# Performance work log

Measured on AMD Instinct MI355X. Metric: run time of the kernel, lower is better.

The kernel has to match this reference:

```python
import jax, jax.numpy as jnp
import numpy as np

N, IN_DIM, HIDDEN, OUT_DIM, K = 16384, 64, 128, 128, 32


def setup_inputs() -> dict:
    key = jax.random.key(0)
    k1, k2, k3 = jax.random.split(key, 3)
    x = jax.random.normal(k1, (N, IN_DIM), dtype=jnp.float32)
    std1 = 1.0 / np.sqrt(2 * IN_DIM)
    w = jax.random.uniform(k2, (HIDDEN, 2 * IN_DIM), dtype=jnp.float32, minval=-std1, maxval=std1)
    std2 = 1.0 / np.sqrt(IN_DIM + HIDDEN)
    w2 = jax.random.uniform(k3, (OUT_DIM, IN_DIM + HIDDEN), dtype=jnp.float32, minval=-std2, maxval=std2)
    return {"x": x, "w": w, "w2": w2, "k": K}


def reference(x, w, w2, k):
    # kNN graph via squared euclidean distances (same ordering as torch.norm cdist)
    sq = jnp.sum(x * x, axis=-1)                      # (N,)
    d2 = sq[:, None] + sq[None, :] - 2.0 * (x @ x.T)  # (N, N)
    _, graph = jax.lax.top_k(-d2, k)                  # (N, k) indices of k smallest distances
    # gather neighbor features and concat broadcast self features
    nb = x[graph]                                      # (N, k, in_dim)
    self_rep = jnp.broadcast_to(x[:, None, :], nb.shape)
    feat = jnp.concatenate([nb, self_rep], axis=-1)    # (N, k, 2*in_dim)
    # linear + Hardtanh + average pooling over neighborhood
    h = jnp.clip(jnp.einsum('nkf,hf->nkh', feat, w), -1.0, 1.0)
    pooled = h.mean(axis=1)                            # (N, hidden)
    # second linear on [pooled, x]
    out = jnp.concatenate([pooled, x], axis=-1) @ w2.T # (N, out_dim)
    return out
```

## Files before the change

### kernel.cpp

```cpp
#include <hip/hip_runtime.h>

#define NPTS   16384
#define IN_DIM 64
#define HID    128
#define KSEL   32

#define CAP    128
#define TRIG   64
#define WIN_HI 48
#define SLACK  0.30f
#define INFBITS 0x7f800000u

typedef _Float16 f16x8 __attribute__((ext_vector_type(8)));
typedef float    f32x4 __attribute__((ext_vector_type(4)));
typedef unsigned short u16;
typedef unsigned int   u32;
typedef unsigned long long u64;

__global__ __launch_bounds__(256) void prep_kernel(const float* __restrict__ x,
                                                   float* __restrict__ sq,
                                                   u16* __restrict__ ph,
                                                   u16* __restrict__ pl) {
    const int i  = blockIdx.x * 256 + threadIdx.x;
    const int ct = i >> 4, li = i & 15;
    const float4* xr = (const float4*)(x + (size_t)i * IN_DIM);
    float s = 0.f;
#pragma unroll
    for (int c = 0; c < 8; ++c) {
        float4 a = xr[2 * c], b = xr[2 * c + 1];
        float e[8] = {a.x, a.y, a.z, a.w, b.x, b.y, b.z, b.w};
        u32 hw[8], lw[8];
#pragma unroll
        for (int j = 0; j < 8; ++j) {
            s += e[j] * e[j];
            _Float16 h = (_Float16)e[j];
            float hf = (float)h;
            _Float16 l = (_Float16)(e[j] - hf);
            hw[j] = __builtin_bit_cast(u16, h);
            lw[j] = __builtin_bit_cast(u16, l);
        }
        size_t off = ((size_t)ct * 8 + c) * 128 + (size_t)li * 8;
        *(uint4*)(ph + off) = make_uint4(hw[0] | (hw[1] << 16), hw[2] | (hw[3] << 16),
                                         hw[4] | (hw[5] << 16), hw[6] | (hw[7] << 16));
        *(uint4*)(pl + off) = make_uint4(lw[0] | (lw[1] << 16), lw[2] | (lw[3] << 16),
                                         lw[4] | (lw[5] << 16), lw[6] | (lw[7] << 16));
    }
    sq[i] = s;
}

__device__ __forceinline__ void compact_row(float* bdrow, u16* bjrow, int* pcnt,
                                            u32* pthr, int lane) {
    int n = *pcnt; n = n < CAP ? n : CAP;
    const float INF = __int_as_float(INFBITS);
    float dv0 = (lane      < n) ? bdrow[lane]      : INF;
    float dv1 = (lane + 64 < n) ? bdrow[lane + 64] : INF;
    u16   jv0 = (lane      < n) ? bjrow[lane]      : 0;
    u16   jv1 = (lane + 64 < n) ? bjrow[lane + 64] : 0;
    u32 u0 = __float_as_uint(dv0), u1 = __float_as_uint(dv1);
    u32 lo = 0, hi = *pthr, ans = hi;
    for (int it = 0; it < 26 && lo < hi; ++it) {
        u32 mid = lo + ((hi - lo) >> 1);
        int c = __popcll(__ballot(u0 <= mid)) + __popcll(__ballot(u1 <= mid));
        if (c < 32) lo = mid + 1;
        else { hi = mid; ans = mid; if (c <= WIN_HI) break; }
    }
    float ansf = __uint_as_float(ans) + SLACK;
    u64 mlt = (1ull << lane) - 1ull;
    bool p0 = dv0 <= ansf;
    u64 b0 = __ballot(p0);
    if (p0) { int p = __popcll(b0 & mlt); bdrow[p] = dv0; bjrow[p] = jv0; }
    int base = __popcll(b0);
    bool p1 = dv1 <= ansf;
    u64 b1 = __ballot(p1);
    if (p1) { int p = base + __popcll(b1 & mlt); if (p < CAP) { bdrow[p] = dv1; bjrow[p] = jv1; } }
    base += __popcll(b1);
    if (lane == 0) {
        *pcnt = base < CAP ? base : CAP;
        atomicMin(pthr, __float_as_uint(ansf));
    }
}

__global__ __launch_bounds__(256, 3) void knn_kernel(const float* __restrict__ x,
                                                     const u16* __restrict__ ph,
                                                     const u16* __restrict__ pl,
                                                     const float* __restrict__ sq,
                                                     int* __restrict__ graph) {
    __shared__ float bd[4][16][CAP];
    __shared__ u16   bj[4][16][CAP];
    __shared__ int   bcnt[4][16];
    __shared__ u32   bthrU[16];

    const int t = threadIdx.x, lane = t & 63, wave = t >> 6;
    const int g = lane >> 4, li = lane & 15;
    const int rg = blockIdx.x;
    const int rbase = rg * 16;

    if (t < 64) bcnt[t >> 4][t & 15] = 0;
    if (t < 16) bthrU[t] = INFBITS;

    f16x8 ah[2], al[2];
#pragma unroll
    for (int kh = 0; kh < 2; ++kh) {
        size_t o = ((size_t)rg * 2 + kh) * 512 + (size_t)lane * 8;
        ah[kh] = *(const f16x8*)(ph + o);
        al[kh] = *(const f16x8*)(pl + o);
    }
    float sar[4];
#pragma unroll
    for (int r = 0; r < 4; ++r) sar[r] = sq[rbase + g * 4 + r];
    __syncthreads();

    int ctb = wave * 4;
    f16x8 cb[4][2]; float csb[4];
#pragma unroll
    for (int c = 0; c < 4; ++c) {
        size_t o = (size_t)(ctb + c) * 1024 + (size_t)lane * 8;
        cb[c][0] = *(const f16x8*)(ph + o);
        cb[c][1] = *(const f16x8*)(ph + o + 512);
        csb[c] = sq[(ctb + c) * 16 + li];
    }

    for (int i = 0; i < 64; ++i) {
        const int nctb = ctb + 16;
        f16x8 nb[4][2]; float nsb[4];
        if (i < 63) {
#pragma unroll
            for (int c = 0; c < 4; ++c) {
                size_t o = (size_t)(nctb + c) * 1024 + (size_t)lane * 8;
                nb[c][0] = *(const f16x8*)(ph + o);
                nb[c][1] = *(const f16x8*)(ph + o + 512);
                nsb[c] = sq[(nctb + c) * 16 + li];
            }
        }
        f32x4 acc[4];
#pragma unroll
        for (int c = 0; c < 4; ++c) {
            f32x4 a = {0.f, 0.f, 0.f, 0.f};
            a = __builtin_amdgcn_mfma_f32_16x16x32_f16(ah[0], cb[c][0], a, 0, 0, 0);
            a = __builtin_amdgcn_mfma_f32_16x16x32_f16(ah[1], cb[c][1], a, 0, 0, 0);
            a = __builtin_amdgcn_mfma_f32_16x16x32_f16(al[0], cb[c][0], a, 0, 0, 0);
            a = __builtin_amdgcn_mfma_f32_16x16x32_f16(al[1], cb[c][1], a, 0, 0, 0);
            acc[c] = a;
        }
        uint4 tu = *(const uint4*)&bthrU[g * 4];
        const float thr[4] = {__uint_as_float(tu.x), __uint_as_float(tu.y),
                              __uint_as_float(tu.z), __uint_as_float(tu.w)};
#pragma unroll
        for (int c = 0; c < 4; ++c) {
#pragma unroll
            for (int r = 0; r < 4; ++r) {
                float d = fmaf(-2.f, acc[c][r], sar[r] + csb[c]);
                bool pred = d <= thr[r];
                if (__any(pred)) {
                    if (pred) {
                        int row = g * 4 + r;
                        int pos = atomicAdd(&bcnt[wave][row], 1);
                        if (pos < CAP) {
                            bd[wave][row][pos] = fmaxf(d, 0.f);
                            bj[wave][row][pos] = (u16)((ctb + c) * 16 + li);
                        }
                    }
                }
            }
        }
        u64 need = __ballot((lane < 16) && (bcnt[wave][lane] > TRIG));
        while (need) {
            int rr = __ffsll((long long)need) - 1;
            need &= need - 1;
            compact_row(bd[wave][rr], bj[wave][rr], &bcnt[wave][rr], &bthrU[rr], lane);
        }
        ctb = nctb;
#pragma unroll
        for (int c = 0; c < 4; ++c) { cb[c][0] = nb[c][0]; cb[c][1] = nb[c][1]; csb[c] = nsb[c]; }
    }

    __syncthreads();

    const u64 mlt = (1ull << lane) - 1ull;
    for (int ii = 0; ii < 4; ++ii) {
        const int lr = wave * 4 + ii;
        const int gr = rbase + lr;
        const float sqa = sq[gr];
        const float4* xa = (const float4*)(x + (size_t)gr * IN_DIM);
        int ns[4];
#pragma unroll
        for (int s = 0; s < 4; ++s) { int v = bcnt[s][lr]; ns[s] = v < CAP ? v : CAP; }
        u32 db[8]; int jj[8];
#pragma unroll
        for (int s8 = 0; s8 < 8; ++s8) {
            const int sl = s8 >> 1;
            const int half = s8 & 1;
            u32 dbits = INFBITS; int j = 0;
            if (ns[sl] > half * 64) {
                int idx = half * 64 + lane;
                if (idx < ns[sl]) {
                    j = bj[sl][lr][idx];
                    const float4* xb = (const float4*)(x + (size_t)j * IN_DIM);
                    float dot = 0.f;
#pragma unroll
                    for (int q = 0; q < 16; ++q) {
                        float4 a = xa[q], b = xb[q];
                        dot += a.x * b.x + a.y * b.y + a.z * b.z + a.w * b.w;
                    }
                    float d = fmaxf(fmaf(-2.f, dot, sqa + sq[j]), 0.f);
                    dbits = __float_as_uint(d);
                }
            }
            db[s8] = dbits; jj[s8] = j;
        }
        u32 lo = 0, hi = INFBITS, ans = hi;
        for (int it = 0; it < 32 && lo < hi; ++it) {
            u32 mid = lo + ((hi - lo) >> 1);
            int c = 0;
#pragma unroll
            for (int s8 = 0; s8 < 8; ++s8)
                c += __popcll(__ballot(db[s8] <= mid));
            if (c < 32) lo = mid + 1;
            else { hi = mid; ans = mid; if (c == 32) break; }
        }
        bool tie[8]; int c_le = 0;
#pragma unroll
        for (int s8 = 0; s8 < 8; ++s8) {
            tie[s8] = (db[s8] == ans);
            c_le += __popcll(__ballot(db[s8] <= ans));
        }
        int extra = c_le - 32;
        while (extra > 0) {
            int mx = -1;
#pragma unroll
            for (int s8 = 0; s8 < 8; ++s8) if (tie[s8] && jj[s8] > mx) mx = jj[s8];
#pragma unroll
            for (int off = 32; off > 0; off >>= 1) {
                int o = __shfl_xor(mx, off); mx = mx > o ? mx : o;
            }
#pragma unroll
            for (int s8 = 0; s8 < 8; ++s8) if (tie[s8] && jj[s8] == mx) tie[s8] = false;
            --extra;
        }
        int* gp = graph + (size_t)gr * KSEL;
        int base = 0;
#pragma unroll
        for (int s8 = 0; s8 < 8; ++s8) {
            bool k = (db[s8] < ans) || tie[s8];
            u64 b = __ballot(k);
            if (k) gp[base + __popcll(b & mlt)] = jj[s8];
            base += __popcll(b);
        }
    }
}

__global__ __launch_bounds__(384) void xw_kernel(const float* __restrict__ x,
                                                 const float* __restrict__ w,
                                                 const float* __restrict__ w2,
                                                 float* __restrict__ XWa,
                                                 float* __restrict__ XWb,
                                                 float* __restrict__ outb) {
    __shared__ float xs[64][64];
    const int t = threadIdx.x;
    const int rbase = blockIdx.x * 64;

    for (int idx = t; idx < 64 * 16; idx += 384) {
        int r = idx >> 4, q = idx & 15;
        ((float4*)xs[r])[q] = ((const float4*)(x + (size_t)(rbase + r) * IN_DIM))[q];
    }
    const int kind = t >> 7;
    const int idx  = t & 127;
    const float* wp = (kind == 0) ? (w + (size_t)idx * 128)
                    : (kind == 1) ? (w + (size_t)idx * 128 + 64)
                                  : (w2 + (size_t)idx * 192 + 128);
    float4 wreg[16];
#pragma unroll
    for (int q = 0; q < 16; ++q) wreg[q] = ((const float4*)wp)[q];
    __syncthreads();

    for (int r = 0; r < 64; ++r) {
        float acc = 0.f;
#pragma unroll
        for (int q = 0; q < 16; ++q) {
            float4 xv = ((float4*)xs[r])[q];
            acc += xv.x * wreg[q].x + xv.y * wreg[q].y +
                   xv.z * wreg[q].z + xv.w * wreg[q].w;
        }
        size_t o = (size_t)(rbase + r) * 128 + idx;
        if (kind == 0)      XWa[o]  = acc;
        else if (kind == 1) XWb[o]  = acc;
        else                outb[o] = acc;
    }
}

__global__ __launch_bounds__(256) void pool_kernel(const int* __restrict__ graph,
                                                   const float* __restrict__ XWa,
                                                   const float* __restrict__ XWb,
                                                   float* __restrict__ pooled) {
    const int t = threadIdx.x, lane = t & 63, wave = t >> 6;
    const int row = blockIdx.x * 4 + wave;
    int gi = graph[(size_t)row * KSEL + (lane & 31)];
    float2 b = ((const float2*)(XWb + (size_t)row * HID))[lane];
    float2 acc = {0.f, 0.f};
#pragma unroll
    for (int c = 0; c < KSEL; ++c) {
        int j = __shfl(gi, c);
        float2 v = ((const float2*)(XWa + (size_t)j * HID))[lane];
        acc.x += fminf(fmaxf(v.x + b.x, -1.f), 1.f);
        acc.y += fminf(fmaxf(v.y + b.y, -1.f), 1.f);
    }
    float2* pr = (float2*)(pooled + (size_t)row * HID);
    pr[lane] = make_float2(acc.x * (1.f / 32.f), acc.y * (1.f / 32.f));
}

__global__ __launch_bounds__(256) void out_kernel(const float* __restrict__ pooled,
                                                  const float* __restrict__ w2,
                                                  float* __restrict__ out) {
    __shared__ float ws2[128][132];
    __shared__ float pt[64][128];
    const int t = threadIdx.x;
    const int rbase = blockIdx.x * 64;

    for (int idx = t; idx < 128 * 32; idx += 256) {
        int o = idx >> 5, q = idx & 31;
        ((float4*)&ws2[o][0])[q] = ((const float4*)(w2 + (size_t)o * 192))[q];
    }
    for (int idx = t; idx < 64 * 32; idx += 256) {
        int r = idx >> 5, q = idx & 31;
        ((float4*)&pt[r][0])[q] = ((const float4*)(pooled + (size_t)(rbase + r) * 128))[q];
    }
    __syncthreads();

    const int o = t & 127, rsub = t >> 7;
    for (int rp = 0; rp < 32; ++rp) {
        int r = rp * 2 + rsub;
        float acc = 0.f;
#pragma unroll
        for (int q = 0; q < 32; ++q) {
            float4 pv = ((float4*)&pt[r][0])[q];
            float4 wv = ((float4*)&ws2[o][0])[q];
            acc += pv.x * wv.x + pv.y * wv.y + pv.z * wv.z + pv.w * wv.w;
        }
        size_t off = (size_t)(rbase + r) * 128 + o;
        out[off] += acc;
    }
}

extern "C" void kernel_launch(void* const* d_in, const int* in_sizes, int n_in,
                              void* d_out, int out_size, void* d_ws, size_t ws_size,
                              hipStream_t stream) {
    const float* x  = (const float*)d_in[0];
    const float* w  = (const float*)d_in[1];
    const float* w2 = (const float*)d_in[2];
    float* out = (float*)d_out;

    float* sq     = (float*)d_ws;
    int*   graph  = (int*)(sq + NPTS);
    float* XWa    = (float*)(graph + (size_t)NPTS * KSEL);
    float* XWb    = XWa + (size_t)NPTS * HID;
    float* region = XWb + (size_t)NPTS * HID;
    u16*   ph     = (u16*)region;
    u16*   pl     = ph + (size_t)NPTS * IN_DIM;
    float* pooled = region;

    prep_kernel<<<NPTS / 256, 256, 0, stream>>>(x, sq, ph, pl);
    knn_kernel<<<NPTS / 16, 256, 0, stream>>>(x, ph, pl, sq, graph);
    xw_kernel<<<NPTS / 64, 384, 0, stream>>>(x, w, w2, XWa, XWb, out);
    pool_kernel<<<NPTS / 4, 256, 0, stream>>>(graph, XWa, XWb, pooled);
    out_kernel<<<NPTS / 64, 256, 0, stream>>>(pooled, w2, out);
}
```

Baseline: 767.6 us.

## Pack kNN candidates as fixed-point distance/index keys and use 8 waves per block

Candidate buffers change from separate float distance and u16 index arrays to a single u32 key holding an 18-bit fixed-point distance and a 14-bit column id. The threshold compare and compaction now run on integers with a single-slot capacity of 64. The block grows to 8 waves, each handling one column tile per iteration instead of four, so per-wave candidate count and LDS per row shrink while occupancy rises. The coarse quantisation and clamping could drop true neighbours if the slack is too small. The final exact float refinement is kept to preserve accuracy.

```diff
diff --git a/kernel.cpp b/kernel.cpp
--- a/kernel.cpp
+++ b/kernel.cpp
@@ -5,17 +5,18 @@
 #define HID    128
 #define KSEL   32
 
-#define CAP    128
-#define TRIG   64
-#define WIN_HI 48
-#define SLACK  0.30f
-#define INFBITS 0x7f800000u
+#define CAP      64
+#define TRIG     48
+#define WIN_HI   44
+#define SLACK_FIX 160u
+#define DMAX_FIX 0x3FFFFu
 
 typedef _Float16 f16x8 __attribute__((ext_vector_type(8)));
 typedef float    f32x4 __attribute__((ext_vector_type(4)));
 typedef unsigned short u16;
 typedef unsigned int   u32;
 typedef unsigned long long u64;
+#define INFBITS 0x7f800000u
 
 __global__ __launch_bounds__(256) void prep_kernel(const float* __restrict__ x,
                                                    float* __restrict__ sq,
@@ -48,55 +49,22 @@
     sq[i] = s;
 }
 
-__device__ __forceinline__ void compact_row(float* bdrow, u16* bjrow, int* pcnt,
-                                            u32* pthr, int lane) {
-    int n = *pcnt; n = n < CAP ? n : CAP;
-    const float INF = __int_as_float(INFBITS);
-    float dv0 = (lane      < n) ? bdrow[lane]      : INF;
-    float dv1 = (lane + 64 < n) ? bdrow[lane + 64] : INF;
-    u16   jv0 = (lane      < n) ? bjrow[lane]      : 0;
-    u16   jv1 = (lane + 64 < n) ? bjrow[lane + 64] : 0;
-    u32 u0 = __float_as_uint(dv0), u1 = __float_as_uint(dv1);
-    u32 lo = 0, hi = *pthr, ans = hi;
-    for (int it = 0; it < 26 && lo < hi; ++it) {
-        u32 mid = lo + ((hi - lo) >> 1);
-        int c = __popcll(__ballot(u0 <= mid)) + __popcll(__ballot(u1 <= mid));
-        if (c < 32) lo = mid + 1;
-        else { hi = mid; ans = mid; if (c <= WIN_HI) break; }
-    }
-    float ansf = __uint_as_float(ans) + SLACK;
-    u64 mlt = (1ull << lane) - 1ull;
-    bool p0 = dv0 <= ansf;
-    u64 b0 = __ballot(p0);
-    if (p0) { int p = __popcll(b0 & mlt); bdrow[p] = dv0; bjrow[p] = jv0; }
-    int base = __popcll(b0);
-    bool p1 = dv1 <= ansf;
-    u64 b1 = __ballot(p1);
-    if (p1) { int p = base + __popcll(b1 & mlt); if (p < CAP) { bdrow[p] = dv1; bjrow[p] = jv1; } }
-    base += __popcll(b1);
-    if (lane == 0) {
-        *pcnt = base < CAP ? base : CAP;
-        atomicMin(pthr, __float_as_uint(ansf));
-    }
-}
-
-__global__ __launch_bounds__(256, 3) void knn_kernel(const float* __restrict__ x,
+__global__ __launch_bounds__(512, 8) void knn_kernel(const float* __restrict__ x,
                                                      const u16* __restrict__ ph,
                                                      const u16* __restrict__ pl,
                                                      const float* __restrict__ sq,
                                                      int* __restrict__ graph) {
-    __shared__ float bd[4][16][CAP];
-    __shared__ u16   bj[4][16][CAP];
-    __shared__ int   bcnt[4][16];
-    __shared__ u32   bthrU[16];
+    __shared__ u32 cand[8][16][CAP];
+    __shared__ int bcnt[8][16];
+    __shared__ u32 bthrU[16];
 
     const int t = threadIdx.x, lane = t & 63, wave = t >> 6;
     const int g = lane >> 4, li = lane & 15;
     const int rg = blockIdx.x;
     const int rbase = rg * 16;
 
-    if (t < 64) bcnt[t >> 4][t & 15] = 0;
-    if (t < 16) bthrU[t] = INFBITS;
+    if (t < 128) bcnt[t >> 4][t & 15] = 0;
+    if (t < 16)  bthrU[t] = 0xffffffffu;
 
     f16x8 ah[2], al[2];
 #pragma unroll
@@ -110,56 +78,44 @@
     for (int r = 0; r < 4; ++r) sar[r] = sq[rbase + g * 4 + r];
     __syncthreads();
 
-    int ctb = wave * 4;
-    f16x8 cb[4][2]; float csb[4];
-#pragma unroll
-    for (int c = 0; c < 4; ++c) {
-        size_t o = (size_t)(ctb + c) * 1024 + (size_t)lane * 8;
-        cb[c][0] = *(const f16x8*)(ph + o);
-        cb[c][1] = *(const f16x8*)(ph + o + 512);
-        csb[c] = sq[(ctb + c) * 16 + li];
-    }
-
-    for (int i = 0; i < 64; ++i) {
-        const int nctb = ctb + 16;
-        f16x8 nb[4][2]; float nsb[4];
-        if (i < 63) {
-#pragma unroll
-            for (int c = 0; c < 4; ++c) {
-                size_t o = (size_t)(nctb + c) * 1024 + (size_t)lane * 8;
-                nb[c][0] = *(const f16x8*)(ph + o);
-                nb[c][1] = *(const f16x8*)(ph + o + 512);
-                nsb[c] = sq[(nctb + c) * 16 + li];
-            }
-        }
-        f32x4 acc[4];
-#pragma unroll
-        for (int c = 0; c < 4; ++c) {
-            f32x4 a = {0.f, 0.f, 0.f, 0.f};
-            a = __builtin_amdgcn_mfma_f32_16x16x32_f16(ah[0], cb[c][0], a, 0, 0, 0);
-            a = __builtin_amdgcn_mfma_f32_16x16x32_f16(ah[1], cb[c][1], a, 0, 0, 0);
-            a = __builtin_amdgcn_mfma_f32_16x16x32_f16(al[0], cb[c][0], a, 0, 0, 0);
-            a = __builtin_amdgcn_mfma_f32_16x16x32_f16(al[1], cb[c][1], a, 0, 0, 0);
-            acc[c] = a;
-        }
+    int ct = wave;
+    f16x8 cb0, cb1; float csb;
+    {
+        size_t o = (size_t)ct * 1024 + (size_t)lane * 8;
+        cb0 = *(const f16x8*)(ph + o);
+        cb1 = *(const f16x8*)(ph + o + 512);
+        csb = sq[ct * 16 + li];
+    }
+
+    for (int i = 0; i < 128; ++i) {
+        const int nct = ct + 8;
+        f16x8 nb0, nb1; float nsb = 0.f;
+        if (i < 127) {
+            size_t o = (size_t)nct * 1024 + (size_t)lane * 8;
+            nb0 = *(const f16x8*)(ph + o);
+            nb1 = *(const f16x8*)(ph + o + 512);
+            nsb = sq[nct * 16 + li];
+        }
+        f32x4 a = {0.f, 0.f, 0.f, 0.f};
+        a = __builtin_amdgcn_mfma_f32_16x16x32_f16(ah[0], cb0, a, 0, 0, 0);
+        a = __builtin_amdgcn_mfma_f32_16x16x32_f16(ah[1], cb1, a, 0, 0, 0);
+        a = __builtin_amdgcn_mfma_f32_16x16x32_f16(al[0], cb0, a, 0, 0, 0);
+        a = __builtin_amdgcn_mfma_f32_16x16x32_f16(al[1], cb1, a, 0, 0, 0);
+
         uint4 tu = *(const uint4*)&bthrU[g * 4];
-        const float thr[4] = {__uint_as_float(tu.x), __uint_as_float(tu.y),
-                              __uint_as_float(tu.z), __uint_as_float(tu.w)};
-#pragma unroll
-        for (int c = 0; c < 4; ++c) {
-#pragma unroll
-            for (int r = 0; r < 4; ++r) {
-                float d = fmaf(-2.f, acc[c][r], sar[r] + csb[c]);
-                bool pred = d <= thr[r];
-                if (__any(pred)) {
-                    if (pred) {
-                        int row = g * 4 + r;
-                        int pos = atomicAdd(&bcnt[wave][row], 1);
-                        if (pos < CAP) {
-                            bd[wave][row][pos] = fmaxf(d, 0.f);
-                            bj[wave][row][pos] = (u16)((ctb + c) * 16 + li);
-                        }
-                    }
+        const u32 thrk[4] = {tu.x, tu.y, tu.z, tu.w};
+        const u32 colid = (u32)(ct * 16 + li);
+#pragma unroll
+        for (int r = 0; r < 4; ++r) {
+            float d = fmaxf(fmaf(-2.f, a[r], sar[r] + csb), 0.f);
+            u32 dfix = (u32)fminf(d * 512.0f, 262143.0f);
+            u32 key = (dfix << 14) | colid;
+            bool pred = key <= thrk[r];
+            if (__any(pred)) {
+                if (pred) {
+                    int row = g * 4 + r;
+                    int pos = atomicAdd(&bcnt[wave][row], 1);
+                    if (pos < CAP) cand[wave][row][pos] = key;
                 }
             }
         }
@@ -167,40 +123,51 @@
         while (need) {
             int rr = __ffsll((long long)need) - 1;
             need &= need - 1;
-            compact_row(bd[wave][rr], bj[wave][rr], &bcnt[wave][rr], &bthrU[rr], lane);
-        }
-        ctb = nctb;
-#pragma unroll
-        for (int c = 0; c < 4; ++c) { cb[c][0] = nb[c][0]; cb[c][1] = nb[c][1]; csb[c] = nsb[c]; }
+            int n = bcnt[wave][rr]; n = n < CAP ? n : CAP;
+            u32 k0 = (lane < n) ? cand[wave][rr][lane] : 0xffffffffu;
+            u32 d0 = k0 >> 14;
+            u32 lo = 0, hi = bthrU[rr] >> 14, ans = hi;
+            for (int it = 0; it < 18 && lo < hi; ++it) {
+                u32 mid = lo + ((hi - lo) >> 1);
+                int c = __popcll(__ballot(d0 <= mid));
+                if (c < 32) lo = mid + 1;
+                else { hi = mid; ans = mid; if (c <= WIN_HI) break; }
+            }
+            u32 ansd = ans + SLACK_FIX; ansd = ansd < DMAX_FIX ? ansd : DMAX_FIX;
+            bool keep = d0 <= ansd;
+            u64 bal = __ballot(keep);
+            int pos = __popcll(bal & ((1ull << lane) - 1ull));
+            if (keep) cand[wave][rr][pos] = k0;
+            if (lane == 0) {
+                bcnt[wave][rr] = __popcll(bal);
+                atomicMin(&bthrU[rr], (ansd << 14) | 0x3fffu);
+            }
+        }
+        ct = nct; cb0 = nb0; cb1 = nb1; csb = nsb;
     }
 
     __syncthreads();
 
     const u64 mlt = (1ull << lane) - 1ull;
-    for (int ii = 0; ii < 4; ++ii) {
-        const int lr = wave * 4 + ii;
+    for (int ii = 0; ii < 2; ++ii) {
+        const int lr = wave * 2 + ii;
         const int gr = rbase + lr;
         const float sqa = sq[gr];
         const float4* xa = (const float4*)(x + (size_t)gr * IN_DIM);
-        int ns[4];
-#pragma unroll
-        for (int s = 0; s < 4; ++s) { int v = bcnt[s][lr]; ns[s] = v < CAP ? v : CAP; }
         u32 db[8]; int jj[8];
 #pragma unroll
         for (int s8 = 0; s8 < 8; ++s8) {
-            const int sl = s8 >> 1;
-            const int half = s8 & 1;
+            int nsl = bcnt[s8][lr]; nsl = nsl < CAP ? nsl : CAP;
             u32 dbits = INFBITS; int j = 0;
-            if (ns[sl] > half * 64) {
-                int idx = half * 64 + lane;
-                if (idx < ns[sl]) {
-                    j = bj[sl][lr][idx];
+            if (nsl > 0) {
+                if (lane < nsl) {
+                    j = (int)(cand[s8][lr][lane] & 0x3fffu);
                     const float4* xb = (const float4*)(x + (size_t)j * IN_DIM);
                     float dot = 0.f;
 #pragma unroll
                     for (int q = 0; q < 16; ++q) {
-                        float4 a = xa[q], b = xb[q];
-                        dot += a.x * b.x + a.y * b.y + a.z * b.z + a.w * b.w;
+                        float4 av = xa[q], bv = xb[q];
+                        dot += av.x * bv.x + av.y * bv.y + av.z * bv.z + av.w * bv.w;
                     }
                     float d = fmaxf(fmaf(-2.f, dot, sqa + sq[j]), 0.f);
                     dbits = __float_as_uint(d);
@@ -359,7 +326,7 @@
     float* pooled = region;
 
     prep_kernel<<<NPTS / 256, 256, 0, stream>>>(x, sq, ph, pl);
-    knn_kernel<<<NPTS / 16, 256, 0, stream>>>(x, ph, pl, sq, graph);
+    knn_kernel<<<NPTS / 16, 512, 0, stream>>>(x, ph, pl, sq, graph);
     xw_kernel<<<NPTS / 64, 384, 0, stream>>>(x, w, w2, XWa, XWb, out);
     pool_kernel<<<NPTS / 4, 256, 0, stream>>>(graph, XWa, XWb, pooled);
     out_kernel<<<NPTS / 64, 256, 0, stream>>>(pooled, w2, out);
```

After: 761.7 us. Within noise of the previous version (-0.8%).
